# Performance work log

Measured on AMD Instinct MI355X. Metric: run time of the kernel, lower is better.

Reference implementation:

```python
import jax, jax.numpy as jnp
import numpy as np

B, S, E, FFN, Q = 8, 2048, 512, 2048, 8


def setup_inputs() -> dict:
    key = jax.random.key(0)
    k0, k1, k2, k3 = jax.random.split(key, 4)
    x = jax.random.normal(k0, (B, S, E), dtype=jnp.float32)
    ry = jax.random.normal(k1, (Q,), dtype=jnp.float32)  # trainable RY angles
    w1 = jax.random.normal(k2, (FFN, Q), dtype=jnp.float32) / np.sqrt(Q).astype(np.float32)
    b1 = jnp.zeros((FFN,), dtype=jnp.float32)
    w2 = jax.random.normal(k3, (E, FFN), dtype=jnp.float32) / np.sqrt(FFN).astype(np.float32)
    b2 = jnp.zeros((E,), dtype=jnp.float32)
    return {"x": x, "ry": ry, "w1": w1, "b1": b1, "w2": w2, "b2": b2}


def reference(x, ry, w1, b1, w2, b2):
    # Quantum layer: each qubit i starts in |0>, gets RX(x[..., i]) then RY(ry[i]),
    # then PauliZ expectation. Product state => closed form <Z_i> = cos(x_i) * cos(ry_i).
    nq = ry.shape[0]
    z = jnp.cos(x[..., :nq]) * jnp.cos(ry)  # [B, S, Q]
    # dropout is identity in eval mode
    h = jnp.einsum("bsq,fq->bsf", z, w1) + b1  # fc1
    return jnp.einsum("bsf,ef->bse", jax.nn.relu(h), w2) + b2  # fc2
```

## Files before the change

kernel.cpp:

```cpp
#include <hip/hip_runtime.h>
#include <cstdint>
#include <cstddef>


typedef __attribute__((ext_vector_type(8))) short s16x8;
typedef __attribute__((ext_vector_type(4))) float f32x4;

__device__ __forceinline__ unsigned short f2bf(float f) {
  unsigned int u = __float_as_uint(f);
  unsigned int r = u + 0x7fffu + ((u >> 16) & 1u);
  return (unsigned short)(r >> 16);
}

__device__ __forceinline__ void async_copy16(const void* g, void* l) {
  __builtin_amdgcn_global_load_lds(
      (const __attribute__((address_space(1))) void*)(uintptr_t)g,
      (__attribute__((address_space(3))) void*)(unsigned int)(uintptr_t)l,
      16, 0, 0);
}

__global__ __launch_bounds__(256) void k_w2(const float* __restrict__ w2,
                                            unsigned short* __restrict__ img) {
  const int n = blockIdx.x;
  const int t = threadIdx.x;
  const int s = t >> 2, quad = t & 3;
  const float* src = w2 + (size_t)n * 2048 + t * 8;
  float4 a = *(const float4*)src;
  float4 b = *(const float4*)(src + 4);
  uint4 pk;
  pk.x = f2bf(a.x) | ((unsigned)f2bf(a.y) << 16);
  pk.y = f2bf(a.z) | ((unsigned)f2bf(a.w) << 16);
  pk.z = f2bf(b.x) | ((unsigned)f2bf(b.y) << 16);
  pk.w = f2bf(b.z) | ((unsigned)f2bf(b.w) << 16);
  const int nt = n >> 8, nl = n & 255, nhi = nl >> 4, nlo = nl & 15;
  const size_t ci = (size_t)(nt * 64 + s) * 1024 + nhi * 64 + quad * 16 + nlo;
  *(uint4*)(img + ci * 8) = pk;
}

__global__ __launch_bounds__(512, 2) void k_fused(
    const float* __restrict__ x, const float* __restrict__ ry,
    const float* __restrict__ w1, const float* __restrict__ b1,
    const unsigned short* __restrict__ w2b, const float* __restrict__ b2,
    float* __restrict__ C) {
  __shared__ unsigned short As[2][128 * 32];
  __shared__ unsigned short Bs[2][256 * 32];
  __shared__ float w1s[2048 * 8];
  __shared__ float b1s[2048];

  const int t = threadIdx.x;
  const int lane = t & 63;
  const int w = t >> 6;
  const int mt = (int)(blockIdx.x >> 1);
  const int nt = (int)(blockIdx.x & 1);
  const int r0 = mt * 128;
  const int c0 = nt * 256;
  const int fp = t & 15;
  const int rq = t >> 4;

  const unsigned short* gB = w2b + (size_t)nt * 64 * 8192 + t * 8;
  char* lB = (char*)Bs + t * 16;
  async_copy16(gB, lB);
  async_copy16(gB + 4096, lB + 8192);
#pragma unroll
  for (int i = 0; i < 8; ++i) {
    const int l = t + i * 512;
    const int sl = l >> 6, wsl = l & 63;
    const int idx = ((wsl & 15) << 2) | (wsl >> 4);
    async_copy16(w1 + (size_t)(sl * 32 + (idx >> 1)) * 8 + (idx & 1) * 4,
                 (char*)w1s + (size_t)l * 16);
  }
  async_copy16(b1 + (size_t)t * 4, (char*)b1s + (size_t)t * 16);
  async_copy16(gB + 8192, lB + 16384);
  async_copy16(gB + 8192 + 4096, lB + 16384 + 8192);

  float zr[4][8];
  {
    float4 ra = *(const float4*)ry;
    float4 rb = *(const float4*)(ry + 4);
    float cy[8] = {__cosf(ra.x), __cosf(ra.y), __cosf(ra.z), __cosf(ra.w),
                   __cosf(rb.x), __cosf(rb.y), __cosf(rb.z), __cosf(rb.w)};
#pragma unroll
    for (int r = 0; r < 4; ++r) {
      const float* xr = x + (size_t)(r0 + rq * 4 + r) * 512;
      float4 x0 = *(const float4*)xr;
      float4 x1 = *(const float4*)(xr + 4);
      zr[r][0] = __cosf(x0.x) * cy[0];
      zr[r][1] = __cosf(x0.y) * cy[1];
      zr[r][2] = __cosf(x0.z) * cy[2];
      zr[r][3] = __cosf(x0.w) * cy[3];
      zr[r][4] = __cosf(x1.x) * cy[4];
      zr[r][5] = __cosf(x1.y) * cy[5];
      zr[r][6] = __cosf(x1.z) * cy[6];
      zr[r][7] = __cosf(x1.w) * cy[7];
    }
  }

  asm volatile("s_waitcnt vmcnt(0) lgkmcnt(0)" ::: "memory");
  __builtin_amdgcn_sched_barrier(0);
  __builtin_amdgcn_s_barrier();

  char* aswr = (char*)As + (rq >> 2) * 1024 +
               (((((fp >> 3) & 1) << 3) | ((rq & 3) << 1) | ((fp >> 2) & 1)) << 4) +
               (fp & 3) * 4;
  auto act = [&](int s, int b) {
    const char* wb = (const char*)w1s + s * 1024 + fp * 16;
    f32x4 v0 = *(const f32x4*)(wb);
    f32x4 v1 = *(const f32x4*)(wb + 256);
    f32x4 v2 = *(const f32x4*)(wb + 512);
    f32x4 v3 = *(const f32x4*)(wb + 768);
    float b0 = b1s[s * 32 + fp * 2];
    float b1v = b1s[s * 32 + fp * 2 + 1];
    char* dst = aswr + b * 8192;
#pragma unroll
    for (int r = 0; r < 4; ++r) {
      float h0 = b0, h1 = b1v;
      h0 += zr[r][0] * v0[0]; h1 += zr[r][0] * v2[0];
      h0 += zr[r][1] * v0[1]; h1 += zr[r][1] * v2[1];
      h0 += zr[r][2] * v0[2]; h1 += zr[r][2] * v2[2];
      h0 += zr[r][3] * v0[3]; h1 += zr[r][3] * v2[3];
      h0 += zr[r][4] * v1[0]; h1 += zr[r][4] * v3[0];
      h0 += zr[r][5] * v1[1]; h1 += zr[r][5] * v3[1];
      h0 += zr[r][6] * v1[2]; h1 += zr[r][6] * v3[2];
      h0 += zr[r][7] * v1[3]; h1 += zr[r][7] * v3[3];
      h0 = fmaxf(h0, 0.0f);
      h1 = fmaxf(h1, 0.0f);
      unsigned int u;
      asm("v_cvt_pk_bf16_f32 %0, %1, %2" : "=v"(u) : "v"(h0), "v"(h1));
      *(unsigned int*)(dst + r * 256) = u;
    }
  };

  act(0, 0);

  const int wm = (w >> 2) * 64;
  const int wn = (w & 3) * 64;
  const int fr = lane & 15;
  const int quad = lane >> 4;

  f32x4 acc[4][4];
#pragma unroll
  for (int i = 0; i < 4; ++i)
#pragma unroll
    for (int j = 0; j < 4; ++j) acc[i][j] = (f32x4){0.f, 0.f, 0.f, 0.f};

  const int slotA = ((fr & 3) << 4) | (((quad >> 1) & 1) << 3) |
                    ((fr >> 2) << 1) | (quad & 1);
  const char* pAb = (const char*)As + ((wm >> 4) * 1024) + slotA * 16;
  const char* pBb = (const char*)Bs + ((wn >> 4) * 1024) + quad * 256 + fr * 16;

  for (int kt = 0; kt < 64; ++kt) {
    const int cur = kt & 1;

    asm volatile("s_waitcnt vmcnt(2) lgkmcnt(0)" ::: "memory");
    __builtin_amdgcn_sched_barrier(0);
    __builtin_amdgcn_s_barrier();

    s16x8 af[4], bfv[4];
    const char* pA = pAb + cur * 8192;
    const char* pB = pBb + cur * 16384;
#pragma unroll
    for (int i = 0; i < 4; ++i) af[i] = *(const s16x8*)(pA + i * 1024);
#pragma unroll
    for (int j = 0; j < 4; ++j) bfv[j] = *(const s16x8*)(pB + j * 1024);

    if (kt < 63) act(kt + 1, cur ^ 1);

    __builtin_amdgcn_s_setprio(1);
#pragma unroll
    for (int i = 0; i < 4; ++i)
#pragma unroll
      for (int j = 0; j < 4; ++j)
        acc[i][j] = __builtin_amdgcn_mfma_f32_16x16x32_bf16(af[i], bfv[j],
                                                            acc[i][j], 0, 0, 0);
    __builtin_amdgcn_s_setprio(0);

    asm volatile("s_waitcnt lgkmcnt(0)" ::: "memory");
    __builtin_amdgcn_sched_barrier(0);
    __builtin_amdgcn_s_barrier();

    if (kt < 62) {
      const unsigned short* g = gB + (size_t)(kt + 2) * 8192;
      char* l = lB + cur * 16384;
      async_copy16(g, l);
      async_copy16(g + 4096, l + 8192);
    }
  }

  float bias[4];
#pragma unroll
  for (int j = 0; j < 4; ++j) bias[j] = b2[c0 + wn + j * 16 + fr];
#pragma unroll
  for (int i = 0; i < 4; ++i) {
    const int rbase = r0 + wm + i * 16 + quad * 4;
#pragma unroll
    for (int rr = 0; rr < 4; ++rr) {
      float* crow = C + (size_t)(rbase + rr) * 512;
#pragma unroll
      for (int j = 0; j < 4; ++j)
        crow[c0 + wn + j * 16 + fr] = acc[i][j][rr] + bias[j];
    }
  }
}

__global__ __launch_bounds__(256) void k_naive(
    const float* __restrict__ x, const float* __restrict__ ry,
    const float* __restrict__ w1, const float* __restrict__ b1,
    const float* __restrict__ w2, const float* __restrict__ b2,
    float* __restrict__ out) {
  __shared__ float zsh[8];
  __shared__ float acts[2048];
  const int r = blockIdx.x;
  const int t = threadIdx.x;
  if (t < 8) zsh[t] = __cosf(x[(size_t)r * 512 + t]) * __cosf(ry[t]);
  __syncthreads();
  float z[8];
#pragma unroll
  for (int q = 0; q < 8; ++q) z[q] = zsh[q];
#pragma unroll
  for (int i = 0; i < 8; ++i) {
    const int f = t * 8 + i;
    const float* wr = w1 + (size_t)f * 8;
    float4 a = *(const float4*)wr;
    float4 b = *(const float4*)(wr + 4);
    float h = b1[f] + z[0] * a.x + z[1] * a.y + z[2] * a.z + z[3] * a.w +
              z[4] * b.x + z[5] * b.y + z[6] * b.z + z[7] * b.w;
    acts[f] = fmaxf(h, 0.0f);
  }
  __syncthreads();
  for (int ee = 0; ee < 2; ++ee) {
    const int e = t + ee * 256;
    const float* wr = w2 + (size_t)e * 2048;
    float acc = b2[e];
    for (int f = 0; f < 2048; f += 4) {
      float4 wv = *(const float4*)(wr + f);
      float4 av = *(const float4*)(acts + f);
      acc += av.x * wv.x + av.y * wv.y + av.z * wv.z + av.w * wv.w;
    }
    out[(size_t)r * 512 + e] = acc;
  }
}

extern "C" void kernel_launch(void* const* d_in, const int* in_sizes, int n_in,
                              void* d_out, int out_size, void* d_ws,
                              size_t ws_size, hipStream_t stream) {
  const float* x  = (const float*)d_in[0];
  const float* ry = (const float*)d_in[1];
  const float* w1 = (const float*)d_in[2];
  const float* b1 = (const float*)d_in[3];
  const float* w2 = (const float*)d_in[4];
  const float* b2 = (const float*)d_in[5];
  float* out = (float*)d_out;

  const size_t w2b_bytes = (size_t)512 * 2048 * 2;
  if (ws_size < w2b_bytes) {
    k_naive<<<dim3(16384), dim3(256), 0, stream>>>(x, ry, w1, b1, w2, b2, out);
    return;
  }
  unsigned short* w2b = (unsigned short*)d_ws;
  k_w2<<<dim3(512), dim3(256), 0, stream>>>(w2, w2b);
  k_fused<<<dim3(256), dim3(512), 0, stream>>>(x, ry, w1, b1, w2b, b2, out);
}
```

Baseline: 148.3 us.

## Halve row tile, drop w1 LDS staging, prefetch w1 into registers

```diff
diff --git a/kernel.cpp b/kernel.cpp
--- a/kernel.cpp
+++ b/kernel.cpp
@@ -37,14 +37,13 @@
   *(uint4*)(img + ci * 8) = pk;
 }
 
-__global__ __launch_bounds__(512, 2) void k_fused(
+__global__ __launch_bounds__(256, 2) void k_fused(
     const float* __restrict__ x, const float* __restrict__ ry,
     const float* __restrict__ w1, const float* __restrict__ b1,
     const unsigned short* __restrict__ w2b, const float* __restrict__ b2,
     float* __restrict__ C) {
-  __shared__ unsigned short As[2][128 * 32];
+  __shared__ unsigned short As[2][64 * 32];
   __shared__ unsigned short Bs[2][256 * 32];
-  __shared__ float w1s[2048 * 8];
   __shared__ float b1s[2048];
 
   const int t = threadIdx.x;
@@ -52,26 +51,10 @@
   const int w = t >> 6;
   const int mt = (int)(blockIdx.x >> 1);
   const int nt = (int)(blockIdx.x & 1);
-  const int r0 = mt * 128;
+  const int r0 = mt * 64;
   const int c0 = nt * 256;
   const int fp = t & 15;
   const int rq = t >> 4;
-
-  const unsigned short* gB = w2b + (size_t)nt * 64 * 8192 + t * 8;
-  char* lB = (char*)Bs + t * 16;
-  async_copy16(gB, lB);
-  async_copy16(gB + 4096, lB + 8192);
-#pragma unroll
-  for (int i = 0; i < 8; ++i) {
-    const int l = t + i * 512;
-    const int sl = l >> 6, wsl = l & 63;
-    const int idx = ((wsl & 15) << 2) | (wsl >> 4);
-    async_copy16(w1 + (size_t)(sl * 32 + (idx >> 1)) * 8 + (idx & 1) * 4,
-                 (char*)w1s + (size_t)l * 16);
-  }
-  async_copy16(b1 + (size_t)t * 4, (char*)b1s + (size_t)t * 16);
-  async_copy16(gB + 8192, lB + 16384);
-  async_copy16(gB + 8192 + 4096, lB + 16384 + 8192);
 
   float zr[4][8];
   {
@@ -94,23 +77,42 @@
       zr[r][7] = __cosf(x1.w) * cy[7];
     }
   }
-
-  asm volatile("s_waitcnt vmcnt(0) lgkmcnt(0)" ::: "memory");
+  __builtin_amdgcn_sched_barrier(0);
+
+  f32x4 wA0, wA1, wA2, wA3, wB0, wB1, wB2, wB3;
+  {
+    const f32x4* p0 = (const f32x4*)(w1 + fp * 16);
+    wA0 = p0[0]; wA1 = p0[1]; wA2 = p0[2]; wA3 = p0[3];
+    const f32x4* p1 = (const f32x4*)(w1 + 256 + fp * 16);
+    wB0 = p1[0]; wB1 = p1[1]; wB2 = p1[2]; wB3 = p1[3];
+  }
+  __builtin_amdgcn_sched_barrier(0);
+
+  const unsigned short* gB = w2b + (size_t)nt * 524288 + t * 8;
+  char* lB = (char*)Bs + t * 16;
+  auto stage = [&](int s, int buf) {
+#pragma unroll
+    for (int p = 0; p < 4; ++p)
+      async_copy16(gB + (size_t)s * 8192 + p * 2048,
+                   lB + buf * 16384 + p * 4096);
+  };
+  stage(0, 0);
+  async_copy16(b1 + (size_t)t * 4, (char*)b1s + (size_t)t * 16);
+  async_copy16(b1 + (size_t)(t + 256) * 4, (char*)b1s + (size_t)(t + 256) * 16);
+  stage(1, 1);
+
+  asm volatile("s_waitcnt vmcnt(4) lgkmcnt(0)" ::: "memory");
   __builtin_amdgcn_sched_barrier(0);
   __builtin_amdgcn_s_barrier();
 
   char* aswr = (char*)As + (rq >> 2) * 1024 +
                (((((fp >> 3) & 1) << 3) | ((rq & 3) << 1) | ((fp >> 2) & 1)) << 4) +
                (fp & 3) * 4;
-  auto act = [&](int s, int b) {
-    const char* wb = (const char*)w1s + s * 1024 + fp * 16;
-    f32x4 v0 = *(const f32x4*)(wb);
-    f32x4 v1 = *(const f32x4*)(wb + 256);
-    f32x4 v2 = *(const f32x4*)(wb + 512);
-    f32x4 v3 = *(const f32x4*)(wb + 768);
+  auto act = [&](int s, int buf, const f32x4& v0, const f32x4& v1,
+                 const f32x4& v2, const f32x4& v3) {
     float b0 = b1s[s * 32 + fp * 2];
     float b1v = b1s[s * 32 + fp * 2 + 1];
-    char* dst = aswr + b * 8192;
+    char* dst = aswr + buf * 4096;
 #pragma unroll
     for (int r = 0; r < 4; ++r) {
       float h0 = b0, h1 = b1v;
@@ -130,40 +132,43 @@
     }
   };
 
-  act(0, 0);
-
-  const int wm = (w >> 2) * 64;
-  const int wn = (w & 3) * 64;
+  act(0, 0, wA0, wA1, wA2, wA3);
+
+  const int wn = w * 64;
   const int fr = lane & 15;
   const int quad = lane >> 4;
-
-  f32x4 acc[4][4];
-#pragma unroll
-  for (int i = 0; i < 4; ++i)
-#pragma unroll
-    for (int j = 0; j < 4; ++j) acc[i][j] = (f32x4){0.f, 0.f, 0.f, 0.f};
-
   const int slotA = ((fr & 3) << 4) | (((quad >> 1) & 1) << 3) |
                     ((fr >> 2) << 1) | (quad & 1);
-  const char* pAb = (const char*)As + ((wm >> 4) * 1024) + slotA * 16;
-  const char* pBb = (const char*)Bs + ((wn >> 4) * 1024) + quad * 256 + fr * 16;
-
-  for (int kt = 0; kt < 64; ++kt) {
+  const char* pAb = (const char*)As + slotA * 16;
+  const char* pBb = (const char*)Bs + w * 4096 + quad * 256 + fr * 16;
+
+  f32x4 acc[4][4];
+#pragma unroll
+  for (int i = 0; i < 4; ++i)
+#pragma unroll
+    for (int j = 0; j < 4; ++j) acc[i][j] = (f32x4){0.f, 0.f, 0.f, 0.f};
+
+  auto body = [&](int kt, const f32x4& u0, const f32x4& u1, const f32x4& u2,
+                  const f32x4& u3, f32x4& l0, f32x4& l1, f32x4& l2,
+                  f32x4& l3) {
+    asm volatile("s_waitcnt vmcnt(4) lgkmcnt(0)" ::: "memory");
+    __builtin_amdgcn_sched_barrier(0);
+    __builtin_amdgcn_s_barrier();
+
+    {
+      const f32x4* p = (const f32x4*)(w1 + (size_t)(kt + 2) * 256 + fp * 16);
+      l0 = p[0]; l1 = p[1]; l2 = p[2]; l3 = p[3];
+    }
     const int cur = kt & 1;
-
-    asm volatile("s_waitcnt vmcnt(2) lgkmcnt(0)" ::: "memory");
-    __builtin_amdgcn_sched_barrier(0);
-    __builtin_amdgcn_s_barrier();
-
     s16x8 af[4], bfv[4];
-    const char* pA = pAb + cur * 8192;
+    const char* pA = pAb + cur * 4096;
     const char* pB = pBb + cur * 16384;
 #pragma unroll
     for (int i = 0; i < 4; ++i) af[i] = *(const s16x8*)(pA + i * 1024);
 #pragma unroll
     for (int j = 0; j < 4; ++j) bfv[j] = *(const s16x8*)(pB + j * 1024);
 
-    if (kt < 63) act(kt + 1, cur ^ 1);
+    act(kt + 1, cur ^ 1, u0, u1, u2, u3);
 
     __builtin_amdgcn_s_setprio(1);
 #pragma unroll
@@ -178,12 +183,53 @@
     __builtin_amdgcn_sched_barrier(0);
     __builtin_amdgcn_s_barrier();
 
-    if (kt < 62) {
-      const unsigned short* g = gB + (size_t)(kt + 2) * 8192;
-      char* l = lB + cur * 16384;
-      async_copy16(g, l);
-      async_copy16(g + 4096, l + 8192);
-    }
+    stage(kt + 2, cur);
+  };
+
+  for (int kt = 0; kt < 62; kt += 2) {
+    body(kt, wB0, wB1, wB2, wB3, wA0, wA1, wA2, wA3);
+    body(kt + 1, wA0, wA1, wA2, wA3, wB0, wB1, wB2, wB3);
+  }
+
+  {
+    asm volatile("s_waitcnt vmcnt(4) lgkmcnt(0)" ::: "memory");
+    __builtin_amdgcn_sched_barrier(0);
+    __builtin_amdgcn_s_barrier();
+    s16x8 af[4], bfv[4];
+#pragma unroll
+    for (int i = 0; i < 4; ++i) af[i] = *(const s16x8*)(pAb + i * 1024);
+#pragma unroll
+    for (int j = 0; j < 4; ++j) bfv[j] = *(const s16x8*)(pBb + j * 1024);
+    act(63, 1, wB0, wB1, wB2, wB3);
+    __builtin_amdgcn_s_setprio(1);
+#pragma unroll
+    for (int i = 0; i < 4; ++i)
+#pragma unroll
+      for (int j = 0; j < 4; ++j)
+        acc[i][j] = __builtin_amdgcn_mfma_f32_16x16x32_bf16(af[i], bfv[j],
+                                                            acc[i][j], 0, 0, 0);
+    __builtin_amdgcn_s_setprio(0);
+    asm volatile("s_waitcnt lgkmcnt(0)" ::: "memory");
+    __builtin_amdgcn_sched_barrier(0);
+    __builtin_amdgcn_s_barrier();
+  }
+  {
+    asm volatile("s_waitcnt vmcnt(0) lgkmcnt(0)" ::: "memory");
+    __builtin_amdgcn_sched_barrier(0);
+    __builtin_amdgcn_s_barrier();
+    s16x8 af[4], bfv[4];
+#pragma unroll
+    for (int i = 0; i < 4; ++i)
+      af[i] = *(const s16x8*)(pAb + 4096 + i * 1024);
+#pragma unroll
+    for (int j = 0; j < 4; ++j)
+      bfv[j] = *(const s16x8*)(pBb + 16384 + j * 1024);
+#pragma unroll
+    for (int i = 0; i < 4; ++i)
+#pragma unroll
+      for (int j = 0; j < 4; ++j)
+        acc[i][j] = __builtin_amdgcn_mfma_f32_16x16x32_bf16(af[i], bfv[j],
+                                                            acc[i][j], 0, 0, 0);
   }
 
   float bias[4];
@@ -191,7 +237,7 @@
   for (int j = 0; j < 4; ++j) bias[j] = b2[c0 + wn + j * 16 + fr];
 #pragma unroll
   for (int i = 0; i < 4; ++i) {
-    const int rbase = r0 + wm + i * 16 + quad * 4;
+    const int rbase = r0 + i * 16 + quad * 4;
 #pragma unroll
     for (int rr = 0; rr < 4; ++rr) {
       float* crow = C + (size_t)(rbase + rr) * 512;
@@ -258,5 +304,5 @@
   }
   unsigned short* w2b = (unsigned short*)d_ws;
   k_w2<<<dim3(512), dim3(256), 0, stream>>>(w2, w2b);
-  k_fused<<<dim3(256), dim3(512), 0, stream>>>(x, ry, w1, b1, w2b, b2, out);
-}
+  k_fused<<<dim3(512), dim3(256), 0, stream>>>(x, ry, w1, b1, w2b, b2, out);
+}
```

Result: no change. 149.9 us (+1.1%).
